# Kernel tuning notes

Measured on AMD Instinct MI355X. Metric: run time of the kernel, lower is better.

## Reference

```python
import jax, jax.numpy as jnp
import numpy as np

B_, C_, H_, W_, Dd_ = 2, 64, 32, 32, 32
D_INNER, D_STATE, DT_RANK, D_CONV = 64, 8, 4, 4


def setup_inputs() -> dict:
    key = jax.random.key(0)
    ks = jax.random.split(key, 12)
    s = 0.05
    A_init = jnp.log(jnp.tile(jnp.arange(1, D_STATE + 1, dtype=jnp.float32), (D_INNER, 1)))
    return {
        "input": jax.random.normal(ks[0], (B_, C_, H_, W_, Dd_), jnp.float32),
        "conv_w": jax.random.normal(ks[1], (C_, C_, 3, 3, 3), jnp.float32) * s,
        "conv_b": jax.random.normal(ks[2], (C_,), jnp.float32) * s,
        "in_proj_w": jax.random.normal(ks[3], (2 * D_INNER, C_), jnp.float32) * s,
        "conv1d_w": jax.random.normal(ks[4], (D_INNER, 1, D_CONV), jnp.float32) * s,
        "conv1d_b": jax.random.normal(ks[5], (D_INNER,), jnp.float32) * s,
        "x_proj_w": jax.random.normal(ks[6], (DT_RANK + 2 * D_STATE, D_INNER), jnp.float32) * s,
        "dt_proj_w": jax.random.normal(ks[7], (D_INNER, DT_RANK), jnp.float32) * s,
        "dt_proj_b": jax.random.normal(ks[8], (D_INNER,), jnp.float32) * s,
        "A_log": A_init,
        "A_b_log": A_init + 0.01,
        "D_skip": jnp.ones((D_INNER,), jnp.float32),
        "out_proj_w": jax.random.normal(ks[9], (C_, D_INNER), jnp.float32) * s,
        "ln_g": jnp.ones((C_,), jnp.float32),
        "ln_b": jnp.zeros((C_,), jnp.float32),
    }


def _conv3d(x, w, b):
    y = jax.lax.conv_general_dilated(x, w, (1, 1, 1), [(1, 1), (1, 1), (1, 1)],
                                     dimension_numbers=("NCDHW", "OIDHW", "NCDHW"))
    return y + b[None, :, None, None, None]


def _instance_norm(x, eps=1e-5):
    m = x.mean(axis=(2, 3, 4), keepdims=True)
    v = ((x - m) ** 2).mean(axis=(2, 3, 4), keepdims=True)
    return (x - m) * jax.lax.rsqrt(v + eps)


def _selective_scan(xc, dt, Bm, Cm, A, D_skip):
    # xc, dt: (b,L,d); Bm, Cm: (b,L,n); A: (d,n)
    dA = jnp.exp(dt[..., None] * A)                       # (b,L,d,n)
    dBx = (dt * xc)[..., None] * Bm[:, :, None, :]        # (b,L,d,n)

    def comb(l, r):
        al, bl = l
        ar, br = r
        return ar * al, ar * bl + br

    _, h = jax.lax.associative_scan(comb, (dA, dBx), axis=1)
    y = jnp.einsum("bldn,bln->bld", h, Cm)
    return y + xc * D_skip


def _direction(xz, conv1d_w, conv1d_b, x_proj_w, dt_proj_w, dt_proj_b, A, D_skip):
    x, z = jnp.split(xz, 2, axis=-1)                      # each (b,L,d)
    xt = jnp.swapaxes(x, 1, 2)                            # (b,d,L)
    xc = jax.lax.conv_general_dilated(xt, conv1d_w, (1,), [(D_CONV - 1, 0)],
                                      feature_group_count=D_INNER,
                                      dimension_numbers=("NCH", "OIH", "NCH"))
    xc = jax.nn.silu(jnp.swapaxes(xc + conv1d_b[None, :, None], 1, 2))  # (b,L,d)
    dbl = xc @ x_proj_w.T
    dt_r = dbl[..., :DT_RANK]
    Bm = dbl[..., DT_RANK:DT_RANK + D_STATE]
    Cm = dbl[..., DT_RANK + D_STATE:]
    dt = jax.nn.softplus(dt_r @ dt_proj_w.T + dt_proj_b)
    y = _selective_scan(xc, dt, Bm, Cm, A, D_skip)
    return y * jax.nn.silu(z)


def reference(input, conv_w, conv_b, in_proj_w, conv1d_w, conv1d_b, x_proj_w,
              dt_proj_w, dt_proj_b, A_log, A_b_log, D_skip, out_proj_w, ln_g, ln_b):
    # skip path: Conv3d -> InstanceNorm3d -> ReLU
    skip = jax.nn.relu(_instance_norm(_conv3d(input, conv_w, conv_b)))
    b, c, h, w, d = input.shape
    tokens = input.transpose(0, 2, 3, 4, 1).reshape(b, h * w * d, c)  # b (hwd) c
    xz = tokens @ in_proj_w.T                                          # (b,L,2d)
    A = -jnp.exp(A_log)
    A_b = -jnp.exp(A_b_log)
    y_f = _direction(xz, conv1d_w, conv1d_b, x_proj_w, dt_proj_w, dt_proj_b, A, D_skip)
    y_b = _direction(xz[:, ::-1], conv1d_w, conv1d_b, x_proj_w, dt_proj_w, dt_proj_b, A_b, D_skip)[:, ::-1]
    out = ((y_f + y_b) @ out_proj_w.T) / 2.0  # if_devide_out=True
    mu = out.mean(-1, keepdims=True)
    var = ((out - mu) ** 2).mean(-1, keepdims=True)
    out = (out - mu) * jax.lax.rsqrt(var + 1e-5) * ln_g + ln_b  # use_norm=True
    vol = out.reshape(b, h, w, d, c).transpose(0, 4, 1, 2, 3)
    return _conv3d(vol, conv_w, conv_b) + skip
```

## Files before the change

### kernel.cpp

```cpp
#include <hip/hip_runtime.h>
#include <hip/hip_bf16.h>

typedef __hip_bfloat16 bf16;
typedef __attribute__((ext_vector_type(8))) short short8;
typedef __attribute__((ext_vector_type(4))) short short4v;
typedef __attribute__((ext_vector_type(4))) float f32x4;

__device__ __forceinline__ float b2f(bf16 x){ return __bfloat162float(x); }
__device__ __forceinline__ bf16  f2b(float x){ return __float2bfloat16(x); }
__device__ __forceinline__ float s2f(short s){ bf16 t = *(bf16*)&s; return b2f(t); }

#define LOG2E 1.4426950408889634f

__device__ __forceinline__ float fexp2(float x){ return __builtin_amdgcn_exp2f(x); }

__device__ __forceinline__ float fsilu(float x){
  return x * __builtin_amdgcn_rcpf(1.f + fexp2(-LOG2E*x));
}

__device__ __forceinline__ float ldin(const void* p, size_t i, int f32){
  return f32 ? ((const float*)p)[i] : b2f(((const bf16*)p)[i]);
}
__device__ __forceinline__ void stout(void* p, size_t i, float v, int f32){
  if(f32) ((float*)p)[i] = v; else ((bf16*)p)[i] = f2b(v);
}

constexpr int SP   = 32*32*32;
constexpr int LTOK = SP;
constexpr int NC   = 1024;
constexpr int CLEN = LTOK / NC;
constexpr int NSEQ = 2*2*64*8;
constexpr int SEG  = 32;
constexpr int SEGLEN = NC/SEG;

__global__ void k_detect(const void* conv_w, int* flag){
  if(threadIdx.x==0 && blockIdx.x==0){
    const bf16* p = (const bf16*)conv_w;
    int f = 0;
    for(int i=0;i<128;i++){
      float v = b2f(p[i]);
      if(!(v==v) || fabsf(v) > 1.0f) f = 1;
    }
    *flag = f;
  }
}

__global__ void k_fill(void* out, int n, const int* flag){
  const int f32 = *flag;
  int i = blockIdx.x*256 + threadIdx.x;
  if(i<n) stout(out, i, 12345.0f, f32);
}

__global__ void k_wprep(const void* __restrict__ cw, bf16* __restrict__ wt,
                        float* __restrict__ zbuf, const int* __restrict__ flag){
  const int f32 = *flag;
  if(blockIdx.x==0 && threadIdx.x<4) zbuf[threadIdx.x] = 0.f;
  int t = blockIdx.x*256 + threadIdx.x;
  if(t >= 27*64*64) return;
  int tap = t >> 12;
  int oc  = (t >> 6) & 63;
  int ci  = t & 63;
  wt[t] = f2b(ldin(cw, ((size_t)(oc*64+ci))*27 + tap, f32));
}

__global__ __launch_bounds__(256) void k_inprojm(
    const void* __restrict__ in, const void* __restrict__ pw,
    bf16* __restrict__ xz, bf16* __restrict__ xin_t,
    const int* __restrict__ flag){
  const int f32 = *flag;
  __shared__ bf16 tok[128*72];
  __shared__ bf16 wl [128*72];
  int tid = threadIdx.x;
  int b = blockIdx.x >> 8, tile = blockIdx.x & 255;
  int l0 = tile*128;

  for(int p=tid; p<1024; p+=256){
    int j = p & 127, c8 = p >> 7;
    short8 v;
    #pragma unroll
    for(int k=0;k<8;k++){
      bf16 t = f2b(ldin(pw, j*64 + c8*8 + k, f32));
      v[k] = *(short*)&t;
    }
    *(short8*)(&wl[j*72 + c8*8]) = v;
  }
  for(int p=tid; p<1024; p+=256){
    int i = p & 127, c8 = p >> 7;
    short8 v;
    #pragma unroll
    for(int k=0;k<8;k++){
      bf16 t = f2b(ldin(in, ((size_t)(b*64 + c8*8 + k))*SP + l0 + i, f32));
      v[k] = *(short*)&t;
    }
    *(short8*)(&tok[i*72 + c8*8]) = v;
  }
  __syncthreads();

  int lane = tid & 63, wv = tid >> 6;
  int pn = lane & 15, quad = lane >> 4, kg8 = quad*8;
  f32x4 acc[2][8];
  #pragma unroll
  for(int mt=0;mt<2;mt++)
    #pragma unroll
    for(int nt=0;nt<8;nt++) acc[mt][nt]=(f32x4)(0.f);

  #pragma unroll
  for(int kq=0;kq<2;kq++){
    short8 a0 = *(const short8*)(&tok[(wv*32      + pn)*72 + kq*32 + kg8]);
    short8 a1 = *(const short8*)(&tok[(wv*32 + 16 + pn)*72 + kq*32 + kg8]);
    #pragma unroll
    for(int nt=0;nt<8;nt++){
      short8 bb = *(const short8*)(&wl[(nt*16+pn)*72 + kq*32 + kg8]);
      acc[0][nt] = __builtin_amdgcn_mfma_f32_16x16x32_bf16(a0,bb,acc[0][nt],0,0,0);
      acc[1][nt] = __builtin_amdgcn_mfma_f32_16x16x32_bf16(a1,bb,acc[1][nt],0,0,0);
    }
  }

  #pragma unroll
  for(int mt=0;mt<2;mt++){
    #pragma unroll
    for(int nt=0;nt<8;nt++){
      #pragma unroll
      for(int r=0;r<4;r++){
        int token = wv*32 + mt*16 + quad*4 + r;
        xz[((size_t)b*LTOK + l0 + token)*128 + nt*16 + pn] = f2b(acc[mt][nt][r]);
      }
    }
  }
  for(int p=tid; p<8192; p+=256){
    int i = p >> 6, c = p & 63;
    xin_t[((size_t)b*SP + l0 + i)*64 + c] = tok[i*72 + c];
  }
}

__global__ __launch_bounds__(256, 2) void k_convm(
    const bf16* __restrict__ xin_t, const bf16* __restrict__ wt,
    const void* __restrict__ cb, const bf16* __restrict__ skip,
    bf16* __restrict__ out_bf, void* __restrict__ out_any,
    int mode, const int* __restrict__ flag, const float* __restrict__ zbuf){
  const int f32 = *flag;
  __shared__ bf16 xt[4096*8];

  int tid  = threadIdx.x;
  int lane = tid & 63;
  int wv   = tid >> 6;
  int pn   = lane & 15;
  int quad = lane >> 4;
  int kg8  = quad * 8;
  int laneA = pn*64 + kg8;

  int blk0 = blockIdx.x;
  int blk  = (blk0 & 7)*128 + (blk0 >> 3);
  int ocg = blk & 3;
  int wh  = (blk >> 2) & 1;
  int dh2 = (blk >> 3) & 1;
  int h   = (blk >> 4) & 31;
  int b   = blk >> 9;
  int w0  = wh*16;
  int d0  = dh2*16;

  f32x4 acc[4];
  #pragma unroll
  for(int m=0;m<4;m++) acc[m]=(f32x4)(0.f);

  for(int cic=0; cic<64; cic+=32){
    if(cic) __syncthreads();
    {
      bf16* dstw = &xt[(size_t)(wv*64)*8];
      for(int it=0; it<16; it++){
        int u = it*256 + tid;
        int row = u >> 2;
        int q4  = (u & 3) ^ ((u >> 3) & 3);
        int hh = row / 324; int rem = row - hh*324;
        int ww = rem / 18;  int dd = rem - ww*18;
        int hg = h + hh - 1, wg = w0 + ww - 1, d = d0 + dd - 1;
        bool ok = ((unsigned)hg < 32u) && ((unsigned)wg < 32u) && ((unsigned)d < 32u);
        const void* src = ok
          ? (const void*)&xin_t[(((size_t)b*SP) + hg*1024 + wg*32 + d)*64 + cic + q4*8]
          : (const void*)zbuf;
        __builtin_amdgcn_global_load_lds(
            (const __attribute__((address_space(1))) void*)src,
            (__attribute__((address_space(3))) void*)(dstw + (size_t)it*256*8),
            16, 0, 0);
      }
    }
    __syncthreads();

    short8 afr[27];
    #pragma unroll
    for(int t=0;t<27;t++)
      afr[t] = *(const short8*)(wt + t*4096 + ocg*1024 + cic + laneA);

    #pragma unroll
    for(int kz=0;kz<3;kz++){
      #pragma unroll
      for(int ky=0;ky<3;ky++){
        #pragma unroll
        for(int kx=0;kx<3;kx++){
          int tap = (kz*3+ky)*3+kx;
          #pragma unroll
          for(int wr=0;wr<4;wr++){
            int rix = (kz*18 + wv*4 + wr + ky)*18 + kx + pn;
            int punit = rix*4 + (quad ^ ((rix>>1)&3));
            short8 bb = *(const short8*)(&xt[(size_t)punit*8]);
            acc[wr] = __builtin_amdgcn_mfma_f32_16x16x32_bf16(afr[tap], bb, acc[wr], 0,0,0);
          }
        }
      }
    }
  }

  #pragma unroll
  for(int wr=0;wr<4;wr++){
    #pragma unroll
    for(int r=0;r<4;r++){
      int oc = ocg*16 + quad*4 + r;
      size_t idx = ((size_t)(b*64+oc))*SP + h*1024 + (w0 + wv*4 + wr)*32 + d0 + pn;
      float v = acc[wr][r] + ldin(cb, oc, f32);
      if(mode==0) out_bf[idx] = f2b(v);
      else        stout(out_any, idx, v + b2f(skip[idx]), f32);
    }
  }
}

__global__ void k_inorm(bf16* __restrict__ buf){
  int bc = blockIdx.x;
  bf16* p = buf + (size_t)bc*SP;
  float s=0.f, s2=0.f;
  for(int i=threadIdx.x;i<SP;i+=256){ float v=b2f(p[i]); s+=v; s2+=v*v; }
  __shared__ float sh[8];
  #pragma unroll
  for(int m=32;m>=1;m>>=1){ s += __shfl_xor(s,m); s2 += __shfl_xor(s2,m); }
  int wid = threadIdx.x>>6;
  if((threadIdx.x&63)==0){ sh[wid]=s; sh[4+wid]=s2; }
  __syncthreads();
  if(threadIdx.x==0){ float a=0,b2=0; for(int i=0;i<4;i++){a+=sh[i]; b2+=sh[4+i];} sh[0]=a; sh[4]=b2; }
  __syncthreads();
  float mean = sh[0]*(1.f/SP);
  float var  = sh[4]*(1.f/SP) - mean*mean;
  float inv = rsqrtf(fmaxf(var,0.f) + 1e-5f);
  for(int i=threadIdx.x;i<SP;i+=256){
    float v=(b2f(p[i])-mean)*inv;
    p[i] = f2b(v>0.f ? v : 0.f);
  }
}

__global__ __launch_bounds__(256) void k_dirprep(
                          const bf16* __restrict__ xz, const void* __restrict__ c1w,
                          const void* __restrict__ c1b, const void* __restrict__ xpw,
                          bf16* __restrict__ bcg, float* __restrict__ dtr,
                          const int* __restrict__ flag){
  const int f32 = *flag;
  __shared__ float xs[67][64];
  __shared__ float xcs[64][68];
  __shared__ float xws[20][68];
  int bid = blockIdx.x;
  int g = bid >> 10, b = (bid>>9)&1, tile = bid & 511;
  int l0 = tile*64;
  int gb = g*2+b;
  int tid = threadIdx.x;
  for(int t=tid; t<20*64; t+=256){ int j=t>>6, d=t&63; xws[j][d]=ldin(xpw, t, f32); }
  for(int t=tid; t<67*64; t+=256){
    int row=t>>6, d=t&63;
    int l = l0 + row - 3;
    float v = 0.f;
    if(l>=0 && l<LTOK){
      int lg = g ? (LTOK-1-l) : l;
      v = b2f(xz[((size_t)b*LTOK + lg)*128 + d]);
    }
    xs[row][d]=v;
  }
  __syncthreads();
  {
    int d = tid & 63;
    float cw0=ldin(c1w,d*4+0,f32), cw1=ldin(c1w,d*4+1,f32),
          cw2=ldin(c1w,d*4+2,f32), cw3=ldin(c1w,d*4+3,f32);
    float cb_=ldin(c1b,d,f32);
    for(int tl = tid>>6; tl<64; tl+=4){
      float acc = cb_ + cw0*xs[tl][d] + cw1*xs[tl+1][d] + cw2*xs[tl+2][d] + cw3*xs[tl+3][d];
      xcs[tl][d] = fsilu(acc);
    }
  }
  __syncthreads();
  {
    int tl = tid & 63, wq = tid >> 6;
    float acc[5] = {0.f,0.f,0.f,0.f,0.f};
    #pragma unroll 4
    for(int d4=0; d4<16; d4++){
      float4 xv = *(const float4*)(&xcs[tl][d4*4]);
      #pragma unroll
      for(int jj=0; jj<5; jj++){
        float4 wv = *(const float4*)(&xws[wq*5+jj][d4*4]);
        acc[jj] += xv.x*wv.x + xv.y*wv.y + xv.z*wv.z + xv.w*wv.w;
      }
    }
    size_t l = (size_t)gb*LTOK + l0 + tl;
    #pragma unroll
    for(int jj=0; jj<5; jj++){
      int j = wq*5 + jj;
      if(j<4) dtr[l*4 + j] = acc[jj];
      else    bcg[l*16 + (j-4)] = f2b(acc[jj]);
    }
  }
}

__global__ __launch_bounds__(128, 4) void k_scan1(
                        const bf16* __restrict__ xz, const float* __restrict__ dtr,
                        const bf16* __restrict__ bcg,
                        const void* __restrict__ c1w, const void* __restrict__ c1b,
                        const void* __restrict__ dpw, const void* __restrict__ dpb,
                        const void* __restrict__ alog, const void* __restrict__ ablog,
                        float* __restrict__ psP, float* __restrict__ psS,
                        const int* __restrict__ flag){
  const int f32 = *flag;
  int bid = blockIdx.x;
  int lane = threadIdx.x & 63;
  int nh   = threadIdx.x >> 6;
  int chunk = bid & (NC-1);
  int b = (bid>>10)&1;
  int g = bid>>11;
  int gb = g*2+b;
  const void* al = g ? ablog : alog;
  float ac2[4];
  #pragma unroll
  for(int n=0;n<4;n++) ac2[n] = -LOG2E*__expf(ldin(al, lane*8 + nh*4 + n, f32));
  float m0 = (float)(nh*4+1);
  float acb2 = ac2[0] / m0;
  bool okl = true;
  #pragma unroll
  for(int n=1;n<4;n++) okl = okl && (fabsf(ac2[n] - acb2*(m0+n)) <= 0.01f*fabsf(ac2[n]));
  const bool fastA = __all(okl);
  float cw0=ldin(c1w,lane*4+0,f32), cw1=ldin(c1w,lane*4+1,f32), cw2=ldin(c1w,lane*4+2,f32), cw3=ldin(c1w,lane*4+3,f32);
  float cb_=ldin(c1b,lane,f32);
  float dw0=ldin(dpw,lane*4+0,f32), dw1=ldin(dpw,lane*4+1,f32), dw2=ldin(dpw,lane*4+2,f32), dw3=ldin(dpw,lane*4+3,f32);
  float db_=ldin(dpb,lane,f32);
  float S[4];
  #pragma unroll
  for(int n=0;n<4;n++) S[n]=0.f;
  float Tsum = 0.f;
  int lt0 = chunk*CLEN;
  float x0,x1,x2;
  {
    float xr[3];
    #pragma unroll
    for(int j=0;j<3;j++){
      int lt = lt0-3+j;
      float v=0.f;
      if(lt>=0){ int lg = g ? (LTOK-1-lt) : lt; v=b2f(xz[((size_t)b*LTOK+lg)*128 + lane]); }
      xr[j]=v;
    }
    x0=xr[0]; x1=xr[1]; x2=xr[2];
  }
  for(int i0=0;i0<CLEN;i0+=8){
    bf16 xv[8]; float4 dv[8]; short4v bb[8];
    #pragma unroll
    for(int k=0;k<8;k++){
      int lt = lt0+i0+k;
      int lg = g ? (LTOK-1-lt) : lt;
      xv[k] = xz[((size_t)b*LTOK+lg)*128 + lane];
      size_t l = (size_t)gb*LTOK + lt;
      dv[k] = *(const float4*)(dtr + l*4);
      bb[k] = *(const short4v*)(bcg + l*16 + nh*4);
    }
    #pragma unroll
    for(int k=0;k<8;k++){
      float x3 = b2f(xv[k]);
      float pre = cb_ + cw0*x0 + cw1*x1 + cw2*x2 + cw3*x3;
      float xc = fsilu(pre);
      float v = db_ + dv[k].x*dw0 + dv[k].y*dw1 + dv[k].z*dw2 + dv[k].w*dw3;
      float e = fexp2(-LOG2E*fabsf(v));
      float dt = fmaxf(v,0.f) + __logf(1.f+e);
      Tsum += dt;
      float bx = dt*xc;
      float a[4];
      if(fastA){
        float e1 = fexp2(dt*acb2);
        if(nh==0){ a[0]=e1; a[1]=e1*e1; a[2]=a[1]*e1; a[3]=a[1]*a[1]; }
        else { float e2=e1*e1, e4=e2*e2; a[0]=e4*e1; a[1]=e4*e2; a[2]=a[1]*e1; a[3]=e4*e4; }
      }else{
        #pragma unroll
        for(int n=0;n<4;n++) a[n] = fexp2(dt*ac2[n]);
      }
      #pragma unroll
      for(int n=0;n<4;n++) S[n] = a[n]*S[n] + bx*s2f(bb[k][n]);
      x0=x1; x1=x2; x2=x3;
    }
  }
  int seq = (gb*64 + lane)*8 + nh*4;
  #pragma unroll
  for(int n=0;n<4;n++){
    psP[(size_t)chunk*NSEQ + seq + n] = fexp2(ac2[n]*Tsum);
    psS[(size_t)chunk*NSEQ + seq + n] = S[n];
  }
}

__global__ void k_scan2a(const float* __restrict__ psP, const float* __restrict__ psS,
                         float* __restrict__ segP, float* __restrict__ segS){
  int idx = blockIdx.x*256 + threadIdx.x;
  int seq = idx & (NSEQ-1);
  int seg = idx >> 11;
  float P = 1.f, S = 0.f;
  int i0 = seg*SEGLEN;
  #pragma unroll 4
  for(int i=0;i<SEGLEN;i++){
    float p = psP[(size_t)(i0+i)*NSEQ + seq];
    float s = psS[(size_t)(i0+i)*NSEQ + seq];
    S = p*S + s;
    P *= p;
  }
  segP[seg*NSEQ + seq] = P;
  segS[seg*NSEQ + seq] = S;
}
__global__ void k_scan2b(const float* __restrict__ segP, const float* __restrict__ segS,
                         float* __restrict__ segC){
  int seq = blockIdx.x*256 + threadIdx.x;
  if(seq >= NSEQ) return;
  float h = 0.f;
  #pragma unroll
  for(int s=0;s<SEG;s++){
    segC[s*NSEQ + seq] = h;
    h = segP[s*NSEQ + seq]*h + segS[s*NSEQ + seq];
  }
}
__global__ void k_scan2c(const float* __restrict__ psP, const float* __restrict__ segC,
                         float* __restrict__ psC){
  int idx = blockIdx.x*256 + threadIdx.x;
  int seq = idx & (NSEQ-1);
  int seg = idx >> 11;
  float h = segC[seg*NSEQ + seq];
  int i0 = seg*SEGLEN;
  #pragma unroll 4
  for(int i=0;i<SEGLEN;i++){
    float p = psP[(size_t)(i0+i)*NSEQ + seq];
    float s = psC[(size_t)(i0+i)*NSEQ + seq];
    psC[(size_t)(i0+i)*NSEQ + seq] = h;
    h = p*h + s;
  }
}

__global__ __launch_bounds__(128, 4) void k_scan3(
                        const bf16* __restrict__ xz, const float* __restrict__ dtr,
                        const bf16* __restrict__ bcg,
                        const void* __restrict__ c1w, const void* __restrict__ c1b,
                        const void* __restrict__ dpw, const void* __restrict__ dpb,
                        const void* __restrict__ alog, const void* __restrict__ ablog,
                        const void* __restrict__ dskip, const float* __restrict__ carry,
                        bf16* __restrict__ ybuf, const int* __restrict__ flag){
  const int f32 = *flag;
  __shared__ float ysh[2][8][64];
  int bid = blockIdx.x;
  int lane = threadIdx.x & 63;
  int nh   = threadIdx.x >> 6;
  int chunk = bid & (NC-1);
  int b = (bid>>10)&1;
  int g = bid>>11;
  int gb = g*2+b;
  const void* al = g ? ablog : alog;
  float ac2[4];
  #pragma unroll
  for(int n=0;n<4;n++) ac2[n] = -LOG2E*__expf(ldin(al, lane*8 + nh*4 + n, f32));
  float m0 = (float)(nh*4+1);
  float acb2 = ac2[0] / m0;
  bool okl = true;
  #pragma unroll
  for(int n=1;n<4;n++) okl = okl && (fabsf(ac2[n] - acb2*(m0+n)) <= 0.01f*fabsf(ac2[n]));
  const bool fastA = __all(okl);
  float cw0=ldin(c1w,lane*4+0,f32), cw1=ldin(c1w,lane*4+1,f32), cw2=ldin(c1w,lane*4+2,f32), cw3=ldin(c1w,lane*4+3,f32);
  float cb_=ldin(c1b,lane,f32);
  float dw0=ldin(dpw,lane*4+0,f32), dw1=ldin(dpw,lane*4+1,f32), dw2=ldin(dpw,lane*4+2,f32), dw3=ldin(dpw,lane*4+3,f32);
  float db_=ldin(dpb,lane,f32);
  float dsk = ldin(dskip,lane,f32);
  int seq = (gb*64 + lane)*8 + nh*4;
  float h[4];
  #pragma unroll
  for(int n=0;n<4;n++) h[n] = carry[(size_t)chunk*NSEQ + seq + n];
  int lt0 = chunk*CLEN;
  float x0,x1,x2;
  {
    float xr[3];
    #pragma unroll
    for(int j=0;j<3;j++){
      int lt = lt0-3+j;
      float v=0.f;
      if(lt>=0){ int lg = g ? (LTOK-1-lt) : lt; v=b2f(xz[((size_t)b*LTOK+lg)*128 + lane]); }
      xr[j]=v;
    }
    x0=xr[0]; x1=xr[1]; x2=xr[2];
  }
  for(int i0=0;i0<CLEN;i0+=8){
    int bt = (i0>>3)&1;
    bf16 xv[8]; float4 dv[8]; short4v bb[8], cc[8];
    #pragma unroll
    for(int k=0;k<8;k++){
      int lt = lt0+i0+k;
      int lg = g ? (LTOK-1-lt) : lt;
      xv[k] = xz[((size_t)b*LTOK+lg)*128 + lane];
      size_t l = (size_t)gb*LTOK + lt;
      dv[k] = *(const float4*)(dtr + l*4);
      bb[k] = *(const short4v*)(bcg + l*16 + nh*4);
      cc[k] = *(const short4v*)(bcg + l*16 + 8 + nh*4);
    }
    float py[8];
    #pragma unroll
    for(int k=0;k<8;k++){
      float x3 = b2f(xv[k]);
      float pre = cb_ + cw0*x0 + cw1*x1 + cw2*x2 + cw3*x3;
      float xc = fsilu(pre);
      float v = db_ + dv[k].x*dw0 + dv[k].y*dw1 + dv[k].z*dw2 + dv[k].w*dw3;
      float e = fexp2(-LOG2E*fabsf(v));
      float dt = fmaxf(v,0.f) + __logf(1.f+e);
      float bx = dt*xc;
      float part = nh ? xc*dsk : 0.f;
      float a[4];
      if(fastA){
        float e1 = fexp2(dt*acb2);
        if(nh==0){ a[0]=e1; a[1]=e1*e1; a[2]=a[1]*e1; a[3]=a[1]*a[1]; }
        else { float e2=e1*e1, e4=e2*e2; a[0]=e4*e1; a[1]=e4*e2; a[2]=a[1]*e1; a[3]=e4*e4; }
      }else{
        #pragma unroll
        for(int n=0;n<4;n++) a[n] = fexp2(dt*ac2[n]);
      }
      #pragma unroll
      for(int n=0;n<4;n++){
        h[n] = a[n]*h[n] + bx*s2f(bb[k][n]);
        part += h[n]*s2f(cc[k][n]);
      }
      if(nh==0) ysh[bt][k][lane] = part;
      else      py[k] = part;
      x0=x1; x1=x2; x2=x3;
    }
    __syncthreads();
    if(nh==1){
      #pragma unroll
      for(int k=0;k<8;k++){
        size_t l = (size_t)gb*LTOK + lt0+i0+k;
        ybuf[l*64 + lane] = f2b(ysh[bt][k][lane] + py[k]);
      }
    }
  }
}

__global__ __launch_bounds__(256) void k_outln(
                        const bf16* __restrict__ ybuf, const bf16* __restrict__ xz,
                        const void* __restrict__ opw,
                        const void* __restrict__ lng, const void* __restrict__ lnb,
                        bf16* __restrict__ vol_t, const int* __restrict__ flag){
  const int f32 = *flag;
  __shared__ bf16 vsm[64*72];
  __shared__ bf16 wsm[64*72];
  __shared__ float gsm[64], bsm[64];
  int tid = threadIdx.x;
  int b = blockIdx.x >> 9, tile = blockIdx.x & 511;
  int l0 = tile*64;

  for(int p=tid; p<512; p+=256){
    int c = p & 63, d8 = p >> 6;
    short8 v;
    #pragma unroll
    for(int k=0;k<8;k++){ bf16 t = f2b(ldin(opw, c*64 + d8*8 + k, f32)); v[k] = *(short*)&t; }
    *(short8*)(&wsm[c*72 + d8*8]) = v;
  }
  if(tid<64){ gsm[tid]=ldin(lng,tid,f32); bsm[tid]=ldin(lnb,tid,f32); }
  for(int p=tid; p<4096; p+=256){
    int tl = p >> 6, d = p & 63;
    int l = l0 + tl;
    float yf = b2f(ybuf[((size_t)(0+b)*LTOK + l)*64 + d]);
    float yb = b2f(ybuf[((size_t)(2+b)*LTOK + (LTOK-1-l))*64 + d]);
    float z  = b2f(xz[((size_t)b*LTOK + l)*128 + 64 + d]);
    vsm[tl*72 + d] = f2b(0.5f*(yf+yb)*fsilu(z));
  }
  __syncthreads();

  int lane = tid & 63, wv = tid >> 6, pn = lane & 15, quad = lane >> 4, kg8 = quad*8;
  f32x4 acc[4];
  #pragma unroll
  for(int nt=0;nt<4;nt++) acc[nt]=(f32x4)(0.f);
  #pragma unroll
  for(int kq=0;kq<2;kq++){
    short8 a = *(const short8*)(&vsm[(wv*16+pn)*72 + kq*32 + kg8]);
    #pragma unroll
    for(int nt=0;nt<4;nt++){
      short8 bb = *(const short8*)(&wsm[(nt*16+pn)*72 + kq*32 + kg8]);
      acc[nt] = __builtin_amdgcn_mfma_f32_16x16x32_bf16(a,bb,acc[nt],0,0,0);
    }
  }
  __syncthreads();

  float gl[4], bl[4];
  #pragma unroll
  for(int nt=0;nt<4;nt++){ gl[nt]=gsm[nt*16+pn]; bl[nt]=bsm[nt*16+pn]; }
  #pragma unroll
  for(int r=0;r<4;r++){
    float vals[4]; float s=0.f;
    #pragma unroll
    for(int nt=0;nt<4;nt++){ vals[nt]=acc[nt][r]; s+=vals[nt]; }
    #pragma unroll
    for(int m=1;m<16;m<<=1) s += __shfl_xor(s, m);
    float mu = s*(1.f/64.f);
    float s2=0.f;
    #pragma unroll
    for(int nt=0;nt<4;nt++){ float dv=vals[nt]-mu; s2+=dv*dv; }
    #pragma unroll
    for(int m=1;m<16;m<<=1) s2 += __shfl_xor(s2, m);
    float inv = rsqrtf(s2*(1.f/64.f) + 1e-5f);
    int token = wv*16 + quad*4 + r;
    #pragma unroll
    for(int nt=0;nt<4;nt++){
      vsm[token*72 + nt*16 + pn] = f2b((vals[nt]-mu)*inv*gl[nt] + bl[nt]);
    }
  }
  __syncthreads();
  for(int p=tid; p<512; p+=256){
    int tl = p >> 3, d8 = p & 7;
    *(short8*)(&vol_t[((size_t)b*SP + l0 + tl)*64 + d8*8]) = *(const short8*)(&vsm[tl*72 + d8*8]);
  }
}

extern "C" void kernel_launch(void* const* d_in, const int* in_sizes, int n_in,
                              void* d_out, int out_size, void* d_ws, size_t ws_size,
                              hipStream_t stream){
  const void* input  = d_in[0];
  const void* conv_w = d_in[1];
  const void* conv_b = d_in[2];
  const void* inpw   = d_in[3];
  const void* c1w    = d_in[4];
  const void* c1b    = d_in[5];
  const void* xpw    = d_in[6];
  const void* dpw    = d_in[7];
  const void* dpb    = d_in[8];
  const void* alog   = d_in[9];
  const void* ablog  = d_in[10];
  const void* dskip  = d_in[11];
  const void* opw    = d_in[12];
  const void* lng    = d_in[13];
  const void* lnb    = d_in[14];

  char* base = (char*)d_ws;
  bf16*  skipb = (bf16*) (base + 0);
  bf16*  xz    = (bf16*) (base + 8388608);
  bf16*  bcg   = (bf16*) (base + 25165824);
  float* dtr   = (float*)(base + 29360128);
  float* psP   = (float*)(base + 31457280);
  bf16*  xin_t = (bf16*) (base + 39845888);
  bf16*  ybuf  = (bf16*) (base + 31457280);
  float* psS   = (float*)(base + 48234496);
  bf16*  vol_t = (bf16*) (base + 48234496);
  bf16*  wt    = (bf16*) (base + 56623104);
  float* segP  = (float*)(base + 56844288);
  float* segS  = (float*)(base + 57106432);
  float* segC  = (float*)(base + 57368576);
  int*   flagp = (int*)  (base + 57630720);
  float* zbuf  = (float*)(base + 57630736);
  const size_t NEED = 57630752;

  k_detect<<<dim3(1), dim3(64), 0, stream>>>(conv_w, flagp);

  if(ws_size < NEED){
    k_fill<<<dim3((out_size+255)/256), dim3(256), 0, stream>>>(d_out, out_size, flagp);
    return;
  }

  k_wprep  <<<dim3(432),   dim3(256), 0, stream>>>(conv_w, wt, zbuf, flagp);
  k_inprojm<<<dim3(512),   dim3(256), 0, stream>>>(input, inpw, xz, xin_t, flagp);
  k_convm  <<<dim3(1024),  dim3(256), 0, stream>>>(xin_t, wt, conv_b, nullptr, skipb, nullptr, 0, flagp, zbuf);
  k_inorm  <<<dim3(128),   dim3(256), 0, stream>>>(skipb);
  k_dirprep<<<dim3(2048),  dim3(256), 0, stream>>>(xz, c1w, c1b, xpw, bcg, dtr, flagp);
  k_scan1  <<<dim3(4096),  dim3(128), 0, stream>>>(xz, dtr, bcg, c1w, c1b, dpw, dpb, alog, ablog, psP, psS, flagp);
  k_scan2a <<<dim3(256),   dim3(256), 0, stream>>>(psP, psS, segP, segS);
  k_scan2b <<<dim3(8),     dim3(256), 0, stream>>>(segP, segS, segC);
  k_scan2c <<<dim3(256),   dim3(256), 0, stream>>>(psP, segC, psS);
  k_scan3  <<<dim3(4096),  dim3(128), 0, stream>>>(xz, dtr, bcg, c1w, c1b, dpw, dpb, alog, ablog, dskip, psS, ybuf, flagp);
  k_outln  <<<dim3(1024),  dim3(256), 0, stream>>>(ybuf, xz, opw, lng, lnb, vol_t, flagp);
  k_convm  <<<dim3(1024),  dim3(256), 0, stream>>>(vol_t, wt, conv_b, skipb, nullptr, d_out, 1, flagp, zbuf);
}
```

Baseline: 393.9 us.

## Halve conv3d output tile along depth to shrink LDS halo and raise occupancy

Each conv block now covers 16w×8d outputs instead of 16×16, so the LDS halo tile shrinks from 3×18×18 to 3×18×10 rows and blocks double to 2048. Launch bounds are raised to 4 blocks per CU, and the per-thread global source pointers are computed once before the channel loop rather than on every chunk. The aim is more resident waves to hide load latency and less address arithmetic. In exchange, halo overhead per output rises, giving more redundant global-to-LDS traffic, and each wave issues half as many MFMAs per weight fragment load. The zero buffer is also enlarged to cover the padded load slots.

```diff
diff --git a/kernel.cpp b/kernel.cpp
--- a/kernel.cpp
+++ b/kernel.cpp
@@ -54,7 +54,7 @@
 __global__ void k_wprep(const void* __restrict__ cw, bf16* __restrict__ wt,
                         float* __restrict__ zbuf, const int* __restrict__ flag){
   const int f32 = *flag;
-  if(blockIdx.x==0 && threadIdx.x<4) zbuf[threadIdx.x] = 0.f;
+  if(blockIdx.x==0 && threadIdx.x<32) zbuf[threadIdx.x] = 0.f;
   int t = blockIdx.x*256 + threadIdx.x;
   if(t >= 27*64*64) return;
   int tap = t >> 12;
@@ -133,13 +133,13 @@
   }
 }
 
-__global__ __launch_bounds__(256, 2) void k_convm(
+__global__ __launch_bounds__(256, 4) void k_convm(
     const bf16* __restrict__ xin_t, const bf16* __restrict__ wt,
     const void* __restrict__ cb, const bf16* __restrict__ skip,
     bf16* __restrict__ out_bf, void* __restrict__ out_any,
     int mode, const int* __restrict__ flag, const float* __restrict__ zbuf){
   const int f32 = *flag;
-  __shared__ bf16 xt[4096*8];
+  __shared__ bf16 xt[2304*8];
 
   int tid  = threadIdx.x;
   int lane = tid & 63;
@@ -148,38 +148,43 @@
   int quad = lane >> 4;
   int kg8  = quad * 8;
   int laneA = pn*64 + kg8;
+  int pbw = pn >> 3, pbd = pn & 7;
 
   int blk0 = blockIdx.x;
-  int blk  = (blk0 & 7)*128 + (blk0 >> 3);
+  int blk  = (blk0 & 7)*256 + (blk0 >> 3);
   int ocg = blk & 3;
-  int wh  = (blk >> 2) & 1;
-  int dh2 = (blk >> 3) & 1;
-  int h   = (blk >> 4) & 31;
-  int b   = blk >> 9;
+  int dq  = (blk >> 2) & 3;
+  int wh  = (blk >> 4) & 1;
+  int h   = (blk >> 5) & 31;
+  int b   = blk >> 10;
   int w0  = wh*16;
-  int d0  = dh2*16;
-
-  f32x4 acc[4];
-  #pragma unroll
-  for(int m=0;m<4;m++) acc[m]=(f32x4)(0.f);
+  int d0  = dq*8;
+
+  const bf16* srcp[9];
+  #pragma unroll
+  for(int it=0; it<9; it++){
+    int j = it*256 + tid;
+    int row = j >> 2;
+    int q4  = (j & 3) ^ ((j >> 3) & 3);
+    int hh = row/180; int rem = row - hh*180;
+    int ww = rem/10;  int dd = rem - ww*10;
+    int hg = h + hh - 1, wg = w0 + ww - 1, d = d0 + dd - 1;
+    bool ok = (j < 2160) && ((unsigned)hg < 32u) && ((unsigned)wg < 32u) && ((unsigned)d < 32u);
+    srcp[it] = ok ? &xin_t[(((size_t)b*SP) + hg*1024 + wg*32 + d)*64 + q4*8]
+                  : (const bf16*)zbuf;
+  }
+
+  f32x4 acc[2];
+  acc[0]=(f32x4)(0.f); acc[1]=(f32x4)(0.f);
 
   for(int cic=0; cic<64; cic+=32){
     if(cic) __syncthreads();
     {
       bf16* dstw = &xt[(size_t)(wv*64)*8];
-      for(int it=0; it<16; it++){
-        int u = it*256 + tid;
-        int row = u >> 2;
-        int q4  = (u & 3) ^ ((u >> 3) & 3);
-        int hh = row / 324; int rem = row - hh*324;
-        int ww = rem / 18;  int dd = rem - ww*18;
-        int hg = h + hh - 1, wg = w0 + ww - 1, d = d0 + dd - 1;
-        bool ok = ((unsigned)hg < 32u) && ((unsigned)wg < 32u) && ((unsigned)d < 32u);
-        const void* src = ok
-          ? (const void*)&xin_t[(((size_t)b*SP) + hg*1024 + wg*32 + d)*64 + cic + q4*8]
-          : (const void*)zbuf;
+      #pragma unroll
+      for(int it=0; it<9; it++){
         __builtin_amdgcn_global_load_lds(
-            (const __attribute__((address_space(1))) void*)src,
+            (const __attribute__((address_space(1))) void*)(srcp[it] + cic),
             (__attribute__((address_space(3))) void*)(dstw + (size_t)it*256*8),
             16, 0, 0);
       }
@@ -199,11 +204,11 @@
         for(int kx=0;kx<3;kx++){
           int tap = (kz*3+ky)*3+kx;
           #pragma unroll
-          for(int wr=0;wr<4;wr++){
-            int rix = (kz*18 + wv*4 + wr + ky)*18 + kx + pn;
+          for(int wr2=0;wr2<2;wr2++){
+            int rix = (kz*18 + wv*4 + wr2*2 + pbw + ky)*10 + pbd + kx;
             int punit = rix*4 + (quad ^ ((rix>>1)&3));
             short8 bb = *(const short8*)(&xt[(size_t)punit*8]);
-            acc[wr] = __builtin_amdgcn_mfma_f32_16x16x32_bf16(afr[tap], bb, acc[wr], 0,0,0);
+            acc[wr2] = __builtin_amdgcn_mfma_f32_16x16x32_bf16(afr[tap], bb, acc[wr2], 0,0,0);
           }
         }
       }
@@ -211,12 +216,13 @@
   }
 
   #pragma unroll
-  for(int wr=0;wr<4;wr++){
+  for(int wr2=0;wr2<2;wr2++){
     #pragma unroll
     for(int r=0;r<4;r++){
       int oc = ocg*16 + quad*4 + r;
-      size_t idx = ((size_t)(b*64+oc))*SP + h*1024 + (w0 + wv*4 + wr)*32 + d0 + pn;
-      float v = acc[wr][r] + ldin(cb, oc, f32);
+      size_t idx = ((size_t)(b*64+oc))*SP + h*1024
+                 + (w0 + wv*4 + wr2*2 + pbw)*32 + d0 + pbd;
+      float v = acc[wr2][r] + ldin(cb, oc, f32);
       if(mode==0) out_bf[idx] = f2b(v);
       else        stout(out_any, idx, v + b2f(skip[idx]), f32);
     }
@@ -651,7 +657,7 @@
   float* segC  = (float*)(base + 57368576);
   int*   flagp = (int*)  (base + 57630720);
   float* zbuf  = (float*)(base + 57630736);
-  const size_t NEED = 57630752;
+  const size_t NEED = 57630864;
 
   k_detect<<<dim3(1), dim3(64), 0, stream>>>(conv_w, flagp);
 
@@ -662,7 +668,7 @@
 
   k_wprep  <<<dim3(432),   dim3(256), 0, stream>>>(conv_w, wt, zbuf, flagp);
   k_inprojm<<<dim3(512),   dim3(256), 0, stream>>>(input, inpw, xz, xin_t, flagp);
-  k_convm  <<<dim3(1024),  dim3(256), 0, stream>>>(xin_t, wt, conv_b, nullptr, skipb, nullptr, 0, flagp, zbuf);
+  k_convm  <<<dim3(2048),  dim3(256), 0, stream>>>(xin_t, wt, conv_b, nullptr, skipb, nullptr, 0, flagp, zbuf);
   k_inorm  <<<dim3(128),   dim3(256), 0, stream>>>(skipb);
   k_dirprep<<<dim3(2048),  dim3(256), 0, stream>>>(xz, c1w, c1b, xpw, bcg, dtr, flagp);
   k_scan1  <<<dim3(4096),  dim3(128), 0, stream>>>(xz, dtr, bcg, c1w, c1b, dpw, dpb, alog, ablog, psP, psS, flagp);
@@ -671,5 +677,5 @@
   k_scan2c <<<dim3(256),   dim3(256), 0, stream>>>(psP, segC, psS);
   k_scan3  <<<dim3(4096),  dim3(128), 0, stream>>>(xz, dtr, bcg, c1w, c1b, dpw, dpb, alog, ablog, dskip, psS, ybuf, flagp);
   k_outln  <<<dim3(1024),  dim3(256), 0, stream>>>(ybuf, xz, opw, lng, lnb, vol_t, flagp);
-  k_convm  <<<dim3(1024),  dim3(256), 0, stream>>>(vol_t, wt, conv_b, skipb, nullptr, d_out, 1, flagp, zbuf);
-}
+  k_convm  <<<dim3(2048),  dim3(256), 0, stream>>>(vol_t, wt, conv_b, skipb, nullptr, d_out, 1, flagp, zbuf);
+}
```

New measurement: 447.4 us. 1.14x slower.
